# Performance work log

Measured on AMD Instinct MI355X. Metric: run time of the kernel, lower is better.

Reference implementation:

```python
import jax, jax.numpy as jnp
import numpy as np

B, T, D, H, E, K = 4, 1024, 1024, 16, 8, 2
HS = D // H
DFF = 4 * D
N = B * T
CAP_MAX = N * K // E  # static upper bound on expert capacity (all tokens non-skip)
SKIP_THR = 0.5
LN_EPS = 1e-5


def _ln(x, g, b):
    m = x.mean(-1, keepdims=True)
    v = x.var(-1, keepdims=True)  # biased, matches torch LayerNorm
    return (x - m) * jax.lax.rsqrt(v + LN_EPS) * g + b


def setup_inputs() -> dict:
    key = jax.random.key(0)
    ks = jax.random.split(key, 20)
    s = 0.02
    nrm = lambda k, shp: jax.random.normal(k, shp, dtype=jnp.float32) * s
    return {
        "x": jax.random.normal(ks[0], (B, T, D), dtype=jnp.float32),
        "noise": jax.random.normal(ks[1], (B, T, E), dtype=jnp.float32),
        "ln1_g": jnp.ones((D,), jnp.float32), "ln1_b": jnp.zeros((D,), jnp.float32),
        "wq": nrm(ks[2], (D, D)), "wk": nrm(ks[3], (D, D)), "wv": nrm(ks[4], (D, D)),
        "w_proj": nrm(ks[5], (D, D)), "b_proj": jnp.zeros((D,), jnp.float32),
        "ln2_g": jnp.ones((D,), jnp.float32), "ln2_b": jnp.zeros((D,), jnp.float32),
        "w_router": nrm(ks[6], (D, E)), "b_router": jnp.zeros((E,), jnp.float32),
        "w_noise": nrm(ks[7], (D, E)), "b_noise": jnp.zeros((E,), jnp.float32),
        "w_skip": nrm(ks[8], (D, 1)), "b_skip": jnp.zeros((1,), jnp.float32),
        "ew1": nrm(ks[9], (E, D, DFF)), "eb1": jnp.zeros((E, DFF), jnp.float32),
        "ew2": nrm(ks[10], (E, DFF, D)), "eb2": jnp.zeros((E, D), jnp.float32),
    }


def _block(x, noise, ln1_g, ln1_b, wq, wk, wv, w_proj, b_proj, ln2_g, ln2_b,
           w_router, b_router, w_noise, b_noise, w_skip, b_skip, ew1, eb1, ew2, eb2):
    # ---- multi-head causal self-attention (dropout is identity in eval) ----
    h = _ln(x, ln1_g, ln1_b)
    q = (h @ wq).reshape(B, T, H, HS)
    k = (h @ wk).reshape(B, T, H, HS)
    v = (h @ wv).reshape(B, T, H, HS)
    # NOTE: original scales by C**-0.5 with C = n_embed (not head_size)
    wei = jnp.einsum("bqhd,bkhd->bhqk", q, k) * (D ** -0.5)
    tril = jnp.tril(jnp.ones((T, T), bool))
    wei = jnp.where(tril, wei, -jnp.inf)
    wei = jax.nn.softmax(wei, axis=-1)
    attn = jnp.einsum("bhqk,bkhd->bqhd", wei, v).reshape(B, T, D)
    x1 = x + attn @ w_proj + b_proj

    # ---- cross-layer sparse MoE with skip routing ----
    h2 = _ln(x1, ln2_g, ln2_b)
    logits = h2 @ w_router + b_router                      # [B,T,E]
    noisy = logits + noise * jax.nn.softplus(h2 @ w_noise + b_noise)
    vals, idx = jax.lax.top_k(noisy, K)                    # [B,T,K]
    sparse = jnp.full_like(noisy, -jnp.inf)
    bi = jnp.arange(B)[:, None, None]
    ti = jnp.arange(T)[None, :, None]
    sparse = sparse.at[bi, ti, idx].set(vals)
    gates = jax.nn.softmax(sparse, axis=-1)                # [B,T,E]
    skip = (jax.nn.sigmoid(h2 @ w_skip + b_skip)[..., 0] > SKIP_THR)  # [B,T]

    fx = h2.reshape(N, D)
    fg = gates.reshape(N, E)
    fi = idx.reshape(N, K)
    nsk = ~skip.reshape(N)                                  # non-skip tokens
    n_ns = nsk.sum()
    capacity = (n_ns * K) // E                              # floor(tokens*K/E * 1.0)

    # per-expert dispatch with first-come capacity truncation (flat-token order)
    mask = (fi[None, :, :] == jnp.arange(E)[:, None, None]).any(-1) & nsk[None, :]  # [E,N]
    rank = jnp.cumsum(mask, axis=1) - 1                     # arrival order among non-skip
    within = mask & (rank < capacity)
    slot = jnp.where(within, rank, CAP_MAX)
    buf = jnp.full((E, CAP_MAX + 1), N, dtype=jnp.int32)
    buf = buf.at[jnp.arange(E)[:, None], slot].set(jnp.arange(N, dtype=jnp.int32)[None, :])
    tok = buf[:, :CAP_MAX]                                  # [E,CAP_MAX] token id or N (pad)
    valid = tok < N

    xp = jnp.concatenate([fx, jnp.zeros((1, D), fx.dtype)], axis=0)
    xin = xp[tok]                                           # [E,CAP_MAX,D]
    mid = jax.nn.relu(jnp.einsum("ecd,edf->ecf", xin, ew1) + eb1[:, None, :])
    yout = jnp.einsum("ecf,efd->ecd", mid, ew2) + eb2[:, None, :]
    gp = jnp.concatenate([fg, jnp.zeros((1, E), fg.dtype)], axis=0)
    gsel = gp[tok, jnp.arange(E)[:, None]]                  # [E,CAP_MAX]
    wout = yout * (gsel * valid)[..., None]

    updates = jnp.zeros((N + 1, D), fx.dtype).at[tok.reshape(-1)].add(wout.reshape(-1, D))[:N]
    moe_out = jnp.where(nsk[:, None], updates, fx).reshape(B, T, D)  # skipped tokens pass ln2(x1) through
    return x1 + moe_out


def reference(x, noise, ln1_g, ln1_b, wq, wk, wv, w_proj, b_proj, ln2_g, ln2_b,
              w_router, b_router, w_noise, b_noise, w_skip, b_skip, ew1, eb1, ew2, eb2):
    return _block(x, noise, ln1_g, ln1_b, wq, wk, wv, w_proj, b_proj, ln2_g, ln2_b,
                  w_router, b_router, w_noise, b_noise, w_skip, b_skip, ew1, eb1, ew2, eb2)
```

## Files before the change

### kernel.cpp

```cpp
#include <hip/hip_runtime.h>
#include <math.h>

#define TOK_N   4096
#define DMODEL  1024
#define NEXP    8
#define DFFD    4096
#define CAPMAX  1024

typedef __bf16 bf16x8 __attribute__((ext_vector_type(8)));
typedef __bf16 bf16x4 __attribute__((ext_vector_type(4)));
typedef float  f32x4  __attribute__((ext_vector_type(4)));

__device__ __forceinline__ f32x4 MFMA16(bf16x8 a, bf16x8 b, f32x4 c){
  return __builtin_amdgcn_mfma_f32_16x16x32_bf16(a, b, c, 0, 0, 0);
}

__device__ __forceinline__ void gl16(const __bf16* g, __bf16* l){
  __builtin_amdgcn_global_load_lds(
      (const __attribute__((address_space(1))) unsigned int*)g,
      (__attribute__((address_space(3))) unsigned int*)l, 16, 0, 0);
}

__device__ __forceinline__ float wave_sum(float x){
  #pragma unroll
  for (int o=32;o;o>>=1) x += __shfl_down(x,o);
  return x;
}

__global__ __launch_bounds__(256) void prep_kernel(
    const float* __restrict__ wq, const float* __restrict__ wk,
    const float* __restrict__ wv, const float* __restrict__ wp,
    __bf16* __restrict__ dh, __bf16* __restrict__ dl,
    const float* __restrict__ x, const float* __restrict__ g1,
    const float* __restrict__ b1, __bf16* __restrict__ hh, __bf16* __restrict__ hl)
{
  __shared__ float smem[64*65];
  int b = blockIdx.x, t = threadIdx.x;
  if (b < 1024){
    int z = b >> 8, rem = b & 255;
    int k0 = (rem >> 4) * 64, n0 = (rem & 15) * 64;
    const float* in = z==0?wq: z==1?wk: z==2?wv: wp;
    __bf16* oh = dh + (size_t)z*DMODEL*DMODEL;
    __bf16* ol = dl + (size_t)z*DMODEL*DMODEL;
    float (*tile)[65] = (float(*)[65])smem;
    #pragma unroll
    for (int i=0;i<4;i++){
      int row = (t>>4) + i*16, col = (t&15)*4;
      float4 f = *(const float4*)&in[(size_t)(k0+row)*DMODEL + n0 + col];
      tile[row][col]=f.x; tile[row][col+1]=f.y; tile[row][col+2]=f.z; tile[row][col+3]=f.w;
    }
    __syncthreads();
    #pragma unroll
    for (int i=0;i<2;i++){
      int c = t + i*256;
      int orow = c>>3, kg = (c&7)*8;
      bf16x8 hv, lv;
      #pragma unroll
      for (int u=0;u<8;u++){
        float xv = tile[kg+u][orow];
        __bf16 hb = (__bf16)xv;
        hv[u]=hb; lv[u]=(__bf16)(xv-(float)hb);
      }
      *(bf16x8*)&oh[(size_t)(n0+orow)*DMODEL + k0 + kg] = hv;
      *(bf16x8*)&ol[(size_t)(n0+orow)*DMODEL + k0 + kg] = lv;
    }
  } else {
    int n = b - 1024;
    float4 v = ((const float4*)(x + (size_t)n*DMODEL))[t];
    float s  = v.x+v.y+v.z+v.w;
    float sq = v.x*v.x+v.y*v.y+v.z*v.z+v.w*v.w;
    s = wave_sum(s); sq = wave_sum(sq);
    int lane = t & 63, wid = t >> 6;
    if (lane==0){ smem[wid]=s; smem[8+wid]=sq; }
    __syncthreads();
    if (t==0){
      float a = smem[0]+smem[1]+smem[2]+smem[3];
      float c = smem[8]+smem[9]+smem[10]+smem[11];
      float mean = a*(1.0f/DMODEL);
      float var  = c*(1.0f/DMODEL) - mean*mean;
      smem[16] = mean; smem[17] = 1.0f/sqrtf(var + 1e-5f);
    }
    __syncthreads();
    float mean = smem[16], rstd = smem[17];
    float4 g4 = ((const float4*)g1)[t];
    float4 b4 = ((const float4*)b1)[t];
    float o_[4];
    o_[0] = (v.x-mean)*rstd*g4.x + b4.x;
    o_[1] = (v.y-mean)*rstd*g4.y + b4.y;
    o_[2] = (v.z-mean)*rstd*g4.z + b4.z;
    o_[3] = (v.w-mean)*rstd*g4.w + b4.w;
    bf16x4 h4, l4;
    #pragma unroll
    for (int i=0;i<4;i++){ __bf16 hb=(__bf16)o_[i]; h4[i]=hb; l4[i]=(__bf16)(o_[i]-(float)hb); }
    *(bf16x4*)&hh[(size_t)n*DMODEL + t*4] = h4;
    *(bf16x4*)&hl[(size_t)n*DMODEL + t*4] = l4;
  }
}

__global__ __launch_bounds__(256) void ln_router_kernel(
    const float* __restrict__ p0, const float* __restrict__ p1,
    const float* __restrict__ xres, const float* __restrict__ bproj,
    const float* __restrict__ g, const float* __restrict__ b,
    __bf16* __restrict__ oh, __bf16* __restrict__ ol, float* __restrict__ out,
    const float* __restrict__ wr, const float* __restrict__ br,
    const float* __restrict__ wn, const float* __restrict__ bn,
    const float* __restrict__ wsk, const float* __restrict__ bsk,
    const float* __restrict__ noise,
    int* __restrict__ idx2, float* __restrict__ gate2, int* __restrict__ nskv)
{
  int n = blockIdx.x, t = threadIdx.x;
  size_t ro = (size_t)n*DMODEL/4 + t;
  float4 a  = ((const float4*)p0)[ro];
  float4 a1 = ((const float4*)p1)[ro];
  float4 xr = ((const float4*)xres)[ro];
  float4 bp = ((const float4*)bproj)[t];
  float4 v;
  v.x = a.x+a1.x+xr.x+bp.x; v.y = a.y+a1.y+xr.y+bp.y;
  v.z = a.z+a1.z+xr.z+bp.z; v.w = a.w+a1.w+xr.w+bp.w;
  float s  = v.x+v.y+v.z+v.w;
  float sq = v.x*v.x+v.y*v.y+v.z*v.z+v.w*v.w;
  s = wave_sum(s); sq = wave_sum(sq);
  __shared__ float r1[4], r2[4];
  __shared__ float mean_s, rstd_s, sk_s;
  int lane = t & 63, wid = t >> 6;
  if (lane==0){ r1[wid]=s; r2[wid]=sq; }
  __syncthreads();
  if (t==0){
    float aa = r1[0]+r1[1]+r1[2]+r1[3];
    float cc = r2[0]+r2[1]+r2[2]+r2[3];
    float mean = aa*(1.0f/DMODEL);
    float var  = cc*(1.0f/DMODEL) - mean*mean;
    mean_s = mean; rstd_s = 1.0f/sqrtf(var + 1e-5f);
  }
  __syncthreads();
  float mean = mean_s, rstd = rstd_s;
  float4 g4 = ((const float4*)g)[t];
  float4 b4 = ((const float4*)b)[t];
  float o_[4];
  o_[0] = (v.x-mean)*rstd*g4.x + b4.x;
  o_[1] = (v.y-mean)*rstd*g4.y + b4.y;
  o_[2] = (v.z-mean)*rstd*g4.z + b4.z;
  o_[3] = (v.w-mean)*rstd*g4.w + b4.w;
  bf16x4 h4, l4;
  #pragma unroll
  for (int i=0;i<4;i++){ __bf16 hb=(__bf16)o_[i]; h4[i]=hb; l4[i]=(__bf16)(o_[i]-(float)hb); }
  *(bf16x4*)&oh[(size_t)n*DMODEL + t*4] = h4;
  *(bf16x4*)&ol[(size_t)n*DMODEL + t*4] = l4;
  int d0 = t*4;
  const float* wrp = wr + (size_t)d0*NEXP;
  const float* wnp = wn + (size_t)d0*NEXP;
  const float* wsp = wsk + d0;
  float vals[17];
  #pragma unroll
  for (int i=0;i<17;i++) vals[i]=0.f;
  #pragma unroll
  for (int i=0;i<4;i++){
    #pragma unroll
    for (int e=0;e<NEXP;e++){
      vals[e]   += o_[i]*wrp[i*NEXP+e];
      vals[8+e] += o_[i]*wnp[i*NEXP+e];
    }
    vals[16] += o_[i]*wsp[i];
  }
  __shared__ float red[4][17];
  #pragma unroll
  for (int i=0;i<17;i++){
    float xx = wave_sum(vals[i]);
    if (lane==0) red[wid][i] = xx;
  }
  __syncthreads();
  if (t==0){
    float noisy[NEXP];
    #pragma unroll
    for (int e=0;e<NEXP;e++){
      float lr = red[0][e]+red[1][e]+red[2][e]+red[3][e] + br[e];
      float pn = red[0][8+e]+red[1][8+e]+red[2][8+e]+red[3][8+e] + bn[e];
      float sp = fmaxf(pn,0.f) + log1pf(expf(-fabsf(pn)));
      noisy[e] = lr + noise[(size_t)n*NEXP + e]*sp;
    }
    float sk = red[0][16]+red[1][16]+red[2][16]+red[3][16] + bsk[0];
    sk_s = sk;
    nskv[n] = (sk <= 0.f) ? 1 : 0;
    int i0=0; float v0=noisy[0];
    #pragma unroll
    for (int e=1;e<NEXP;e++) if (noisy[e] > v0){ v0=noisy[e]; i0=e; }
    int i1=-1; float v1=-INFINITY;
    #pragma unroll
    for (int e=0;e<NEXP;e++) if (e!=i0 && noisy[e] > v1){ v1=noisy[e]; i1=e; }
    float tt = expf(v1 - v0);
    idx2[n*2+0]=i0; idx2[n*2+1]=i1;
    gate2[n*2+0]=1.0f/(1.0f+tt); gate2[n*2+1]=tt/(1.0f+tt);
  }
  __syncthreads();
  if (sk_s > 0.f){
    v.x += o_[0]; v.y += o_[1]; v.z += o_[2]; v.w += o_[3];
  }
  ((float4*)out)[ro] = v;
}

__global__ __launch_bounds__(256) void tconv_pair(
    const float* __restrict__ ew1, const float* __restrict__ ew2,
    __bf16* __restrict__ e1T, __bf16* __restrict__ e2T, int e0)
{
  __shared__ float tile[64][65];
  int z = blockIdx.z, t = threadIdx.x;
  const float* in; __bf16* out; int K, N, k0, n0;
  if (z < 2){
    in = ew1 + (size_t)(e0+z)*DMODEL*DFFD; out = e1T + (size_t)z*DFFD*DMODEL;
    K = DMODEL; N = DFFD; k0 = blockIdx.y*64; n0 = blockIdx.x*64;
  } else {
    in = ew2 + (size_t)(e0+z-2)*DFFD*DMODEL; out = e2T + (size_t)(z-2)*DMODEL*DFFD;
    K = DFFD; N = DMODEL; k0 = blockIdx.x*64; n0 = blockIdx.y*64;
  }
  #pragma unroll
  for (int i=0;i<4;i++){
    int row = (t>>4) + i*16, col = (t&15)*4;
    float4 f = *(const float4*)&in[(size_t)(k0+row)*N + n0 + col];
    tile[row][col]=f.x; tile[row][col+1]=f.y; tile[row][col+2]=f.z; tile[row][col+3]=f.w;
  }
  __syncthreads();
  #pragma unroll
  for (int i=0;i<2;i++){
    int c = t + i*256;
    int orow = c>>3, kg = (c&7)*8;
    bf16x8 hv;
    #pragma unroll
    for (int u=0;u<8;u++) hv[u] = (__bf16)tile[kg+u][orow];
    *(bf16x8*)&out[(size_t)(n0+orow)*K + k0 + kg] = hv;
  }
}

__global__ __launch_bounds__(256) void btrans_kernel(
    const __bf16* __restrict__ ih, const __bf16* __restrict__ il, int istride, int icol0,
    __bf16* __restrict__ oh, __bf16* __restrict__ ol){
  __shared__ __bf16 th[64][72], tl[64][72];
  int r0 = blockIdx.x*64, c0 = blockIdx.y*64;
  int t = threadIdx.x;
  {
    int r = t>>2, cg = (t&3)*16;
    size_t go = (size_t)(r0+r)*istride + icol0 + c0 + cg;
    *(bf16x8*)&th[r][cg]   = *(const bf16x8*)&ih[go];
    *(bf16x8*)&th[r][cg+8] = *(const bf16x8*)&ih[go+8];
    *(bf16x8*)&tl[r][cg]   = *(const bf16x8*)&il[go];
    *(bf16x8*)&tl[r][cg+8] = *(const bf16x8*)&il[go+8];
  }
  __syncthreads();
  {
    int c = t>>2, rg = (t&3)*16;
    bf16x8 a,b,e,f;
    #pragma unroll
    for (int u=0;u<8;u++){ a[u]=th[rg+u][c]; b[u]=th[rg+8+u][c]; e[u]=tl[rg+u][c]; f[u]=tl[rg+8+u][c]; }
    size_t go = (size_t)(c0+c)*TOK_N + r0 + rg;
    *(bf16x8*)&oh[go]   = a;
    *(bf16x8*)&oh[go+8] = b;
    *(bf16x8*)&ol[go]   = e;
    *(bf16x8*)&ol[go+8] = f;
  }
}

template<int MODE, bool SPLIT>
__global__ __launch_bounds__(256) void mgemm(
    const __bf16* __restrict__ Ah, const __bf16* __restrict__ Al, int Astride,
    const __bf16* __restrict__ Bh, const __bf16* __restrict__ Bl, int Bstride,
    const float* __restrict__ bias,
    float* __restrict__ Cf, __bf16* __restrict__ Ch, __bf16* __restrict__ Cl,
    int N, int K,
    const int* __restrict__ tok, const __bf16* __restrict__ zbuf)
{
  if constexpr (MODE==2){
    int z = blockIdx.z;
    Bh  += (size_t)z*((size_t)DFFD*DMODEL);
    bias+= (size_t)z*DFFD;
    Ch  += (size_t)z*((size_t)CAPMAX*DFFD);
    tok += z*CAPMAX;
  }
  if constexpr (MODE==4){
    int pe = blockIdx.z>>2, kz = blockIdx.z&3;
    Ah  += (size_t)pe*((size_t)CAPMAX*DFFD) + kz*1024;
    Bh  += (size_t)pe*((size_t)DMODEL*DFFD) + kz*1024;
    Cf  += (size_t)blockIdx.z*((size_t)CAPMAX*DMODEL);
    tok += pe*CAPMAX;
  }
  if constexpr (MODE==5){
    int kz = blockIdx.z;
    Ah += kz*512; Al += kz*512; Bh += kz*512; Bl += kz*512;
    Cf += (size_t)kz*((size_t)TOK_N*DMODEL);
  }
  int m0 = blockIdx.y*128, n0 = blockIdx.x*128;
  if ((MODE==2||MODE==4) && tok[m0] >= TOK_N) return;
  __shared__ __align__(16) __bf16 sAh[2*128*32], sBh[2*128*32];
  __shared__ __align__(16) __bf16 sAl[SPLIT?2*128*32:8], sBl[SPLIT?2*128*32:8];
  int t = threadIdx.x, lane = t&63, w = t>>6;
  int wr = w>>1, wc = w&1, fr = lane&15, kb = lane>>4;

  const __bf16* aB[2]; const __bf16* aBl[2]; bool aval[2];
  const __bf16* bB[2]; const __bf16* bBl[2];
  #pragma unroll
  for (int j=0;j<2;j++){
    int c = j*256 + w*64 + lane;
    int row = c>>2, grp = c&3;
    int sg = grp ^ ((row>>1)&3);
    if (MODE==2){
      int token = tok[m0+row];
      if (token < TOK_N){ aB[j] = Ah + (size_t)token*Astride + sg*8; aval[j]=true; }
      else              { aB[j] = zbuf + sg*8;                       aval[j]=false; }
    } else {
      aB[j] = Ah + (size_t)(m0+row)*Astride + sg*8; aval[j]=true;
      if (SPLIT) aBl[j] = Al + (size_t)(m0+row)*Astride + sg*8;
    }
    bB[j] = Bh + (size_t)(n0+row)*Bstride + sg*8;
    if (SPLIT) bBl[j] = Bl + (size_t)(n0+row)*Bstride + sg*8;
  }

  auto stage = [&](int buf, int kt){
    int base = buf*(128*32);
    #pragma unroll
    for (int j=0;j<2;j++){
      int cb8 = base + (j*256 + w*64)*8;
      gl16(aB[j] + (aval[j]? kt : 0), &sAh[cb8]);
      gl16(bB[j] + kt, &sBh[cb8]);
      if constexpr (SPLIT){
        gl16(aBl[j] + kt, &sAl[cb8]);
        gl16(bBl[j] + kt, &sBl[cb8]);
      }
    }
  };

  f32x4 acc[4][4];
  #pragma unroll
  for (int mt=0;mt<4;mt++)
    #pragma unroll
    for (int nt=0;nt<4;nt++) acc[mt][nt] = (f32x4){0.f,0.f,0.f,0.f};

  stage(0, 0);
  __syncthreads();
  int nk = K >> 5;
  int xk = (kb ^ ((fr>>1)&3))*8;
  for (int ik=0; ik<nk; ik++){
    int cur = ik & 1;
    if (ik+1 < nk) stage(cur^1, (ik+1)<<5);
    int fb = cur*(128*32);
    bf16x8 aFh[4], bFh[4];
    #pragma unroll
    for (int mt=0;mt<4;mt++) aFh[mt] = *(const bf16x8*)&sAh[fb + (wr*64+mt*16+fr)*32 + xk];
    #pragma unroll
    for (int nt=0;nt<4;nt++) bFh[nt] = *(const bf16x8*)&sBh[fb + (wc*64+nt*16+fr)*32 + xk];
    __builtin_amdgcn_s_setprio(1);
    #pragma unroll
    for (int mt=0;mt<4;mt++)
      #pragma unroll
      for (int nt=0;nt<4;nt++)
        acc[mt][nt] = MFMA16(aFh[mt], bFh[nt], acc[mt][nt]);
    __builtin_amdgcn_s_setprio(0);
    if constexpr (SPLIT){
      bf16x8 aFl[4], bFl[4];
      #pragma unroll
      for (int mt=0;mt<4;mt++) aFl[mt] = *(const bf16x8*)&sAl[fb + (wr*64+mt*16+fr)*32 + xk];
      #pragma unroll
      for (int nt=0;nt<4;nt++) bFl[nt] = *(const bf16x8*)&sBl[fb + (wc*64+nt*16+fr)*32 + xk];
      __builtin_amdgcn_s_setprio(1);
      #pragma unroll
      for (int mt=0;mt<4;mt++)
        #pragma unroll
        for (int nt=0;nt<4;nt++){
          acc[mt][nt] = MFMA16(aFh[mt], bFl[nt], acc[mt][nt]);
          acc[mt][nt] = MFMA16(aFl[mt], bFh[nt], acc[mt][nt]);
        }
      __builtin_amdgcn_s_setprio(0);
    }
    __syncthreads();
  }

  #pragma unroll
  for (int mt=0; mt<4; mt++){
    int r0 = m0 + wr*64 + mt*16 + (lane>>4)*4;
    #pragma unroll
    for (int nt=0; nt<4; nt++){
      int col = n0 + wc*64 + nt*16 + fr;
      f32x4 v = acc[mt][nt];
      if constexpr (MODE==0){
        #pragma unroll
        for (int jj=0;jj<4;jj++){
          float val = v[jj];
          __bf16 hb = (__bf16)val;
          size_t idx = (size_t)(r0+jj)*N + col;
          Ch[idx] = hb; Cl[idx] = (__bf16)(val-(float)hb);
        }
      } else if constexpr (MODE==2){
        float bs = bias[col];
        #pragma unroll
        for (int jj=0;jj<4;jj++)
          Ch[(size_t)(r0+jj)*N + col] = (__bf16)fmaxf(v[jj]+bs, 0.f);
      } else {
        #pragma unroll
        for (int jj=0;jj<4;jj++)
          Cf[(size_t)(r0+jj)*N + col] = v[jj];
      }
    }
  }
}

__global__ __launch_bounds__(256) void sred_kernel(const float* __restrict__ yk,
    const int* __restrict__ tok, const float* __restrict__ gsel,
    const float* __restrict__ eb2, float* __restrict__ out)
{
  int r = blockIdx.x, t = threadIdx.x;
  int token = tok[r];
  if (token >= TOK_N) return;
  float g = gsel[r];
  float4 acc = ((const float4*)eb2)[t];
  #pragma unroll
  for (int z=0;z<4;z++){
    float4 p = ((const float4*)(yk + (size_t)z*CAPMAX*DMODEL + (size_t)r*DMODEL))[t];
    acc.x+=p.x; acc.y+=p.y; acc.z+=p.z; acc.w+=p.w;
  }
  float* op = out + (size_t)token*DMODEL;
  float4 o = ((float4*)op)[t];
  o.x += g*acc.x; o.y += g*acc.y; o.z += g*acc.z; o.w += g*acc.w;
  ((float4*)op)[t] = o;
}

__global__ __launch_bounds__(256) void attn_mfma_kernel(
    const __bf16* __restrict__ qkvh, const __bf16* __restrict__ qkvl,
    const __bf16* __restrict__ vth, const __bf16* __restrict__ vtl,
    __bf16* __restrict__ oh, __bf16* __restrict__ ol)
{
  __shared__ __align__(16) __bf16 Kh[2][64*64], Kl[2][64*64], Vh[2][64*64], Vl[2][64*64];
  __shared__ __align__(16) __bf16 Pt[2][4][16*64];
  int qtA = blockIdx.x, qtB = qtA + 8;
  int bh = blockIdx.y;
  int batch = bh>>4, head = bh&15;
  int t = threadIdx.x, lane = t&63, w = t>>6;
  int g = lane>>4, fr = lane&15;
  int col0 = head*64;
  size_t qbaseA = (size_t)(batch*1024 + qtA*64);
  size_t qbaseB = (size_t)(batch*1024 + qtB*64);
  const int QKS = 3*DMODEL;
  const float scale = 0.03125f;

  bf16x8 bQhA[2], bQlA[2], bQhB[2], bQlB[2];
  {
    int qrow = w*16 + fr;
    size_t rbA = (qbaseA+qrow)*QKS + col0 + g*8;
    size_t rbB = (qbaseB+qrow)*QKS + col0 + g*8;
    bQhA[0] = *(const bf16x8*)&qkvh[rbA];
    bQhA[1] = *(const bf16x8*)&qkvh[rbA+32];
    bQlA[0] = *(const bf16x8*)&qkvl[rbA];
    bQlA[1] = *(const bf16x8*)&qkvl[rbA+32];
    bQhB[0] = *(const bf16x8*)&qkvh[rbB];
    bQhB[1] = *(const bf16x8*)&qkvh[rbB+32];
    bQlB[0] = *(const bf16x8*)&qkvl[rbB];
    bQlB[1] = *(const bf16x8*)&qkvl[rbB+32];
  }

  auto stageKV = [&](int buf, int kt){
    size_t kbase = (size_t)(batch*1024 + kt*64);
    #pragma unroll
    for (int j=0;j<2;j++){
      int c = j*256 + t, row = c>>3, seg = c&7;
      int lb = (j*256 + w*64)*8;
      size_t gk = (kbase+row)*QKS + 1024 + col0 + ((seg^(row&7))*8);
      gl16(qkvh+gk, &Kh[buf][lb]);
      gl16(qkvl+gk, &Kl[buf][lb]);
      size_t gv = (size_t)(col0+row)*TOK_N + kbase + ((seg^(row&7))*8);
      gl16(vth+gv, &Vh[buf][lb]);
      gl16(vtl+gv, &Vl[buf][lb]);
    }
  };

  float mA = -INFINITY, lA = 0.f, mB = -INFINITY, lB = 0.f;
  f32x4 oA[4], oB[4];
  #pragma unroll
  for (int nt=0;nt<4;nt++){ oA[nt]=(f32x4){0.f,0.f,0.f,0.f}; oB[nt]=(f32x4){0.f,0.f,0.f,0.f}; }

  auto process = [&](int cur, bool diag, bf16x8* bQh, bf16x8* bQl,
                     float& m_, float& l_, f32x4* o_){
    int ntmax = diag ? (w+1) : 4;
    f32x4 s[4];
    #pragma unroll
    for (int nt=0;nt<4;nt++) s[nt]=(f32x4){0.f,0.f,0.f,0.f};
    __builtin_amdgcn_s_setprio(1);
    #pragma unroll
    for (int ks=0; ks<2; ks++){
      #pragma unroll
      for (int nt=0; nt<4; nt++){
        if (nt < ntmax){
          int kvr = nt*16 + fr;
          int sc_ = (ks*4 + g) ^ (kvr&7);
          bf16x8 aKh = *(const bf16x8*)&Kh[cur][kvr*64 + sc_*8];
          bf16x8 aKl = *(const bf16x8*)&Kl[cur][kvr*64 + sc_*8];
          s[nt] = MFMA16(aKh, bQh[ks], s[nt]);
          s[nt] = MFMA16(aKl, bQh[ks], s[nt]);
          s[nt] = MFMA16(aKh, bQl[ks], s[nt]);
        }
      }
    }
    __builtin_amdgcn_s_setprio(0);
    float sv[4][4];
    float mx = -INFINITY;
    int ql = w*16 + fr;
    #pragma unroll
    for (int nt=0;nt<4;nt++)
      #pragma unroll
      for (int j=0;j<4;j++){
        float xv = s[nt][j]*scale;
        if (nt >= ntmax || (diag && (nt*16 + g*4 + j) > ql)) xv = -INFINITY;
        sv[nt][j] = xv;
        mx = fmaxf(mx, xv);
      }
    mx = fmaxf(mx, __shfl_xor(mx,16));
    mx = fmaxf(mx, __shfl_xor(mx,32));
    float nm = fmaxf(m_, mx);
    float scf = __expf(m_ - nm);
    float ps = 0.f;
    #pragma unroll
    for (int nt=0;nt<4;nt++)
      #pragma unroll
      for (int j=0;j<4;j++){
        float p = __expf(sv[nt][j] - nm);
        sv[nt][j] = p;
        ps += p;
      }
    ps += __shfl_xor(ps,16);
    ps += __shfl_xor(ps,32);
    l_ = l_*scf + ps;
    m_ = nm;
    #pragma unroll
    for (int nt=0;nt<4;nt++) o_[nt] = o_[nt]*scf;
    #pragma unroll
    for (int nt=0;nt<4;nt++){
      bf16x4 hv, lv;
      #pragma unroll
      for (int j=0;j<4;j++){
        float pv = sv[nt][j];
        __bf16 hb = (__bf16)pv;
        hv[j] = hb; lv[j] = (__bf16)(pv-(float)hb);
      }
      int el = fr*64 + (((2*nt + (g>>1)) ^ (fr&7))*8) + (g&1)*4;
      *(bf16x4*)&Pt[0][w][el] = hv;
      *(bf16x4*)&Pt[1][w][el] = lv;
    }
    int ksmax = (diag && w < 2) ? 1 : 2;
    __builtin_amdgcn_s_setprio(1);
    #pragma unroll
    for (int ks=0; ks<2; ks++){
      if (ks < ksmax){
        int pc = (4*ks + g) ^ (fr&7);
        bf16x8 bPh = *(const bf16x8*)&Pt[0][w][fr*64 + pc*8];
        bf16x8 bPl = *(const bf16x8*)&Pt[1][w][fr*64 + pc*8];
        #pragma unroll
        for (int nt=0; nt<4; nt++){
          int vr = nt*16 + fr;
          int vc = (ks*4 + g) ^ (vr&7);
          bf16x8 aVh = *(const bf16x8*)&Vh[cur][vr*64 + vc*8];
          bf16x8 aVl = *(const bf16x8*)&Vl[cur][vr*64 + vc*8];
          o_[nt] = MFMA16(aVh, bPh, o_[nt]);
          o_[nt] = MFMA16(aVl, bPh, o_[nt]);
          o_[nt] = MFMA16(aVh, bPl, o_[nt]);
        }
      }
    }
    __builtin_amdgcn_s_setprio(0);
  };

  stageKV(0, 0);
  for (int kt=0; kt<=qtB; kt++){
    int cur = kt&1;
    __syncthreads();
    if (kt < qtB) stageKV(cur^1, kt+1);
    if (kt <= qtA) process(cur, kt==qtA, bQhA, bQlA, mA, lA, oA);
    process(cur, kt==qtB, bQhB, bQlB, mB, lB, oB);
  }

  auto writeOut = [&](size_t qbase, float l_, f32x4* o_){
    float inv = 1.0f/l_;
    #pragma unroll
    for (int nt=0;nt<4;nt++){
      bf16x4 hv, lv;
      #pragma unroll
      for (int j=0;j<4;j++){
        float val = o_[nt][j]*inv;
        __bf16 hb = (__bf16)val;
        hv[j] = hb; lv[j] = (__bf16)(val-(float)hb);
      }
      int el = fr*64 + (((2*nt + (g>>1)) ^ (fr&7))*8) + (g&1)*4;
      *(bf16x4*)&Pt[0][w][el] = hv;
      *(bf16x4*)&Pt[1][w][el] = lv;
    }
    #pragma unroll
    for (int r=0;r<2;r++){
      int c = r*4 + g;
      int el = fr*64 + ((c ^ (fr&7))*8);
      bf16x8 vh = *(const bf16x8*)&Pt[0][w][el];
      bf16x8 vl = *(const bf16x8*)&Pt[1][w][el];
      size_t go = (qbase + w*16 + fr)*DMODEL + col0 + c*8;
      *(bf16x8*)&oh[go] = vh;
      *(bf16x8*)&ol[go] = vl;
    }
  };
  writeOut(qbaseA, lA, oA);
  writeOut(qbaseB, lB, oB);
}

__global__ __launch_bounds__(256) void scan_kernel(const int* __restrict__ idx2,
    const float* __restrict__ gate2, const int* __restrict__ nskv,
    int* __restrict__ tok, float* __restrict__ gsel, float* __restrict__ zbuf)
{
  int t = threadIdx.x;
  for (int i=t; i<NEXP*CAPMAX; i+=256){ tok[i]=TOK_N; gsel[i]=0.f; }
  for (int i=t; i<1024; i+=256) zbuf[i]=0.f;
  __shared__ int cnts[256][NEXP];
  __shared__ int nns_part[256];
  __shared__ int cap_s;
  int loc[NEXP];
  #pragma unroll
  for (int e=0;e<NEXP;e++) loc[e]=0;
  int nn=0, base = t*16;
  for (int u=0;u<16;u++){
    int n = base+u;
    if (nskv[n]){ nn++; loc[idx2[n*2]]++; loc[idx2[n*2+1]]++; }
  }
  #pragma unroll
  for (int e=0;e<NEXP;e++) cnts[t][e]=loc[e];
  nns_part[t]=nn;
  __syncthreads();
  if (t < NEXP){ int run=0; for (int i=0;i<256;i++){ int c=cnts[i][t]; cnts[i][t]=run; run+=c; } }
  if (t == NEXP){ int sum=0; for (int i=0;i<256;i++) sum+=nns_part[i]; cap_s = sum/4; }
  __syncthreads();
  int capacity = cap_s;
  int run[NEXP];
  #pragma unroll
  for (int e=0;e<NEXP;e++) run[e]=cnts[t][e];
  for (int u=0;u<16;u++){
    int n = base+u;
    if (!nskv[n]) continue;
    #pragma unroll
    for (int kk=0;kk<2;kk++){
      int e = idx2[n*2+kk];
      int r = run[e]++;
      if (r < capacity){ tok[e*CAPMAX+r]=n; gsel[e*CAPMAX+r]=gate2[n*2+kk]; }
    }
  }
}

extern "C" void kernel_launch(void* const* d_in, const int* in_sizes, int n_in,
                              void* d_out, int out_size, void* d_ws, size_t ws_size,
                              hipStream_t stream) {
  const float* x      = (const float*)d_in[0];
  const float* noise  = (const float*)d_in[1];
  const float* ln1_g  = (const float*)d_in[2];
  const float* ln1_b  = (const float*)d_in[3];
  const float* wq     = (const float*)d_in[4];
  const float* wk     = (const float*)d_in[5];
  const float* wv     = (const float*)d_in[6];
  const float* w_proj = (const float*)d_in[7];
  const float* b_proj = (const float*)d_in[8];
  const float* ln2_g  = (const float*)d_in[9];
  const float* ln2_b  = (const float*)d_in[10];
  const float* w_rout = (const float*)d_in[11];
  const float* b_rout = (const float*)d_in[12];
  const float* w_noi  = (const float*)d_in[13];
  const float* b_noi  = (const float*)d_in[14];
  const float* w_skip = (const float*)d_in[15];
  const float* b_skip = (const float*)d_in[16];
  const float* ew1    = (const float*)d_in[17];
  const float* eb1    = (const float*)d_in[18];
  const float* ew2    = (const float*)d_in[19];
  const float* eb2    = (const float*)d_in[20];
  float* out = (float*)d_out;

  char* ws = (char*)d_ws;
  const size_t MB = 1024*1024;
  __bf16* h_hi   = (__bf16*)(ws + 0*MB);
  __bf16* h_lo   = (__bf16*)(ws + 8*MB);
  __bf16* qkv_hi = (__bf16*)(ws + 16*MB);
  __bf16* qkv_lo = (__bf16*)(ws + 40*MB);
  __bf16* wAllT_h= (__bf16*)(ws + 64*MB);
  __bf16* wAllT_l= (__bf16*)(ws + 72*MB);
  __bf16* vt_hi  = (__bf16*)(ws + 81*MB);
  __bf16* vt_lo  = (__bf16*)(ws + 89*MB);
  float*  pP     = (float*) (ws + 16*MB);
  int*   idx2  = (int*)  (ws + 96*MB);
  float* gate2 = (float*)(ws + 96*MB + 32*1024);
  int*   nskv  = (int*)  (ws + 96*MB + 64*1024);
  int*   tokb  = (int*)  (ws + 96*MB + 80*1024);
  float* gselb = (float*)(ws + 96*MB + 112*1024);
  float* zbuf  = (float*)(ws + 96*MB + 144*1024);
  __bf16* e1T_2 = (__bf16*)(ws + 16*MB);
  __bf16* e2T_2 = (__bf16*)(ws + 32*MB);
  __bf16* mid_2 = (__bf16*)(ws + 48*MB);
  float*  yk    = (float*) (ws + 64*MB);
  __bf16* ao_hi = h_hi, *ao_lo = h_lo;

  dim3 blk(256);
  prep_kernel<<<5120, blk, 0, stream>>>(wq, wk, wv, w_proj, wAllT_h, wAllT_l,
                                        x, ln1_g, ln1_b, h_hi, h_lo);
  mgemm<0,true><<<dim3(24,32), blk, 0, stream>>>(h_hi, h_lo, DMODEL, wAllT_h, wAllT_l, DMODEL,
      nullptr, nullptr, qkv_hi, qkv_lo, 3*DMODEL, DMODEL, nullptr, nullptr);
  btrans_kernel<<<dim3(64,16), blk, 0, stream>>>(qkv_hi, qkv_lo, 3*DMODEL, 2048, vt_hi, vt_lo);
  attn_mfma_kernel<<<dim3(8,64), blk, 0, stream>>>(qkv_hi, qkv_lo, vt_hi, vt_lo, ao_hi, ao_lo);
  mgemm<5,true><<<dim3(8,32,2), blk, 0, stream>>>(ao_hi, ao_lo, DMODEL,
      wAllT_h + (size_t)3*DMODEL*DMODEL, wAllT_l + (size_t)3*DMODEL*DMODEL, DMODEL,
      nullptr, pP, nullptr, nullptr, DMODEL, 512, nullptr, nullptr);
  ln_router_kernel<<<TOK_N, blk, 0, stream>>>(pP, pP + (size_t)TOK_N*DMODEL, x, b_proj,
      ln2_g, ln2_b, h_hi, h_lo, out,
      w_rout, b_rout, w_noi, b_noi, w_skip, b_skip, noise, idx2, gate2, nskv);
  scan_kernel<<<1, blk, 0, stream>>>(idx2, gate2, nskv, tokb, gselb, zbuf);
  for (int p=0; p<4; p++){
    int e0 = 2*p;
    tconv_pair<<<dim3(64,16,4), blk, 0, stream>>>(ew1, ew2, e1T_2, e2T_2, e0);
    mgemm<2,false><<<dim3(32,8,2), blk, 0, stream>>>(h_hi, nullptr, DMODEL,
        e1T_2, nullptr, DMODEL, eb1 + (size_t)e0*DFFD,
        nullptr, mid_2, nullptr, DFFD, DMODEL, tokb + e0*CAPMAX, (const __bf16*)zbuf);
    mgemm<4,false><<<dim3(8,8,8), blk, 0, stream>>>(mid_2, nullptr, DFFD,
        e2T_2, nullptr, DFFD, nullptr,
        yk, nullptr, nullptr, DMODEL, 1024, tokb + e0*CAPMAX, nullptr);
    for (int pe=0; pe<2; pe++){
      int e = e0 + pe;
      sred_kernel<<<CAPMAX, blk, 0, stream>>>(yk + (size_t)pe*4*CAPMAX*DMODEL,
          tokb + e*CAPMAX, gselb + e*CAPMAX, eb2 + (size_t)e*DMODEL, out);
    }
  }
}
```

Baseline: 606.3 us.

## Process experts in larger groups and replace per-expert scatter with per-token gather

Expert processing is batched into groups of up to 8 experts, chosen from the available workspace size, so that the weight transpose, the two expert GEMMs and the reduction each run with wider grids and fewer launches. The scan kernel now also records, for each token, which expert slots it occupies. A per-token gather kernel replaces the per-expert scatter kernels, reading the split-K partials and adding gated outputs in one read-modify-write of each output row. Larger groups need much more workspace, and the gather launches one block per token even when most tokens are absent from the current group.

```diff
diff --git a/kernel.cpp b/kernel.cpp
--- a/kernel.cpp
+++ b/kernel.cpp
@@ -198,18 +198,18 @@
   ((float4*)out)[ro] = v;
 }
 
-__global__ __launch_bounds__(256) void tconv_pair(
+__global__ __launch_bounds__(256) void tconv_group(
     const float* __restrict__ ew1, const float* __restrict__ ew2,
-    __bf16* __restrict__ e1T, __bf16* __restrict__ e2T, int e0)
+    __bf16* __restrict__ e1T, __bf16* __restrict__ e2T, int e0, int G)
 {
   __shared__ float tile[64][65];
   int z = blockIdx.z, t = threadIdx.x;
   const float* in; __bf16* out; int K, N, k0, n0;
-  if (z < 2){
+  if (z < G){
     in = ew1 + (size_t)(e0+z)*DMODEL*DFFD; out = e1T + (size_t)z*DFFD*DMODEL;
     K = DMODEL; N = DFFD; k0 = blockIdx.y*64; n0 = blockIdx.x*64;
   } else {
-    in = ew2 + (size_t)(e0+z-2)*DFFD*DMODEL; out = e2T + (size_t)(z-2)*DMODEL*DFFD;
+    in = ew2 + (size_t)(e0+z-G)*DFFD*DMODEL; out = e2T + (size_t)(z-G)*DMODEL*DFFD;
     K = DFFD; N = DMODEL; k0 = blockIdx.x*64; n0 = blockIdx.y*64;
   }
   #pragma unroll
@@ -275,11 +275,11 @@
     tok += z*CAPMAX;
   }
   if constexpr (MODE==4){
-    int pe = blockIdx.z>>2, kz = blockIdx.z&3;
-    Ah  += (size_t)pe*((size_t)CAPMAX*DFFD) + kz*1024;
-    Bh  += (size_t)pe*((size_t)DMODEL*DFFD) + kz*1024;
+    int ge = blockIdx.z>>2, kz = blockIdx.z&3;
+    Ah  += (size_t)ge*((size_t)CAPMAX*DFFD) + kz*1024;
+    Bh  += (size_t)ge*((size_t)DMODEL*DFFD) + kz*1024;
     Cf  += (size_t)blockIdx.z*((size_t)CAPMAX*DMODEL);
-    tok += pe*CAPMAX;
+    tok += ge*CAPMAX;
   }
   if constexpr (MODE==5){
     int kz = blockIdx.z;
@@ -400,24 +400,32 @@
   }
 }
 
-__global__ __launch_bounds__(256) void sred_kernel(const float* __restrict__ yk,
-    const int* __restrict__ tok, const float* __restrict__ gsel,
-    const float* __restrict__ eb2, float* __restrict__ out)
+__global__ __launch_bounds__(256) void gather_kernel(const float* __restrict__ yk,
+    const int* __restrict__ tsrc, const float* __restrict__ gselb,
+    const float* __restrict__ eb2, int e0, int G, float* __restrict__ out)
 {
-  int r = blockIdx.x, t = threadIdx.x;
-  int token = tok[r];
-  if (token >= TOK_N) return;
-  float g = gsel[r];
-  float4 acc = ((const float4*)eb2)[t];
-  #pragma unroll
-  for (int z=0;z<4;z++){
-    float4 p = ((const float4*)(yk + (size_t)z*CAPMAX*DMODEL + (size_t)r*DMODEL))[t];
-    acc.x+=p.x; acc.y+=p.y; acc.z+=p.z; acc.w+=p.w;
-  }
-  float* op = out + (size_t)token*DMODEL;
-  float4 o = ((float4*)op)[t];
-  o.x += g*acc.x; o.y += g*acc.y; o.z += g*acc.z; o.w += g*acc.w;
-  ((float4*)op)[t] = o;
+  int n = blockIdx.x, t = threadIdx.x;
+  int s0 = tsrc[n*2], s1 = tsrc[n*2+1];
+  float4 o; bool any = false;
+  #pragma unroll
+  for (int kk=0; kk<2; kk++){
+    int src = kk ? s1 : s0;
+    if (src < 0) continue;
+    int e = src >> 10;
+    int ge = e - e0;
+    if (ge < 0 || ge >= G) continue;
+    int r = src & (CAPMAX-1);
+    if (!any){ o = ((const float4*)(out + (size_t)n*DMODEL))[t]; any = true; }
+    float g = gselb[src];
+    float4 acc = ((const float4*)(eb2 + (size_t)e*DMODEL))[t];
+    #pragma unroll
+    for (int z=0; z<4; z++){
+      float4 p = ((const float4*)(yk + ((size_t)(ge*4+z)*CAPMAX + r)*DMODEL))[t];
+      acc.x+=p.x; acc.y+=p.y; acc.z+=p.z; acc.w+=p.w;
+    }
+    o.x += g*acc.x; o.y += g*acc.y; o.z += g*acc.z; o.w += g*acc.w;
+  }
+  if (any) ((float4*)(out + (size_t)n*DMODEL))[t] = o;
 }
 
 __global__ __launch_bounds__(256) void attn_mfma_kernel(
@@ -604,10 +612,12 @@
 
 __global__ __launch_bounds__(256) void scan_kernel(const int* __restrict__ idx2,
     const float* __restrict__ gate2, const int* __restrict__ nskv,
-    int* __restrict__ tok, float* __restrict__ gsel, float* __restrict__ zbuf)
+    int* __restrict__ tok, float* __restrict__ gsel, float* __restrict__ zbuf,
+    int* __restrict__ tsrc)
 {
   int t = threadIdx.x;
   for (int i=t; i<NEXP*CAPMAX; i+=256){ tok[i]=TOK_N; gsel[i]=0.f; }
+  for (int i=t; i<2*TOK_N; i+=256) tsrc[i] = -1;
   for (int i=t; i<1024; i+=256) zbuf[i]=0.f;
   __shared__ int cnts[256][NEXP];
   __shared__ int nns_part[256];
@@ -638,7 +648,10 @@
     for (int kk=0;kk<2;kk++){
       int e = idx2[n*2+kk];
       int r = run[e]++;
-      if (r < capacity){ tok[e*CAPMAX+r]=n; gsel[e*CAPMAX+r]=gate2[n*2+kk]; }
+      if (r < capacity){
+        tok[e*CAPMAX+r]=n; gsel[e*CAPMAX+r]=gate2[n*2+kk];
+        tsrc[n*2+kk] = e*CAPMAX + r;
+      }
     }
   }
 }
@@ -680,17 +693,28 @@
   __bf16* vt_hi  = (__bf16*)(ws + 81*MB);
   __bf16* vt_lo  = (__bf16*)(ws + 89*MB);
   float*  pP     = (float*) (ws + 16*MB);
-  int*   idx2  = (int*)  (ws + 96*MB);
-  float* gate2 = (float*)(ws + 96*MB + 32*1024);
-  int*   nskv  = (int*)  (ws + 96*MB + 64*1024);
-  int*   tokb  = (int*)  (ws + 96*MB + 80*1024);
-  float* gselb = (float*)(ws + 96*MB + 112*1024);
-  float* zbuf  = (float*)(ws + 96*MB + 144*1024);
-  __bf16* e1T_2 = (__bf16*)(ws + 16*MB);
-  __bf16* e2T_2 = (__bf16*)(ws + 32*MB);
-  __bf16* mid_2 = (__bf16*)(ws + 48*MB);
-  float*  yk    = (float*) (ws + 64*MB);
   __bf16* ao_hi = h_hi, *ao_lo = h_lo;
+
+  int G; size_t off_mid, off_yk, off_e1, off_e2, off_meta;
+  if (ws_size >= (size_t)338*MB){
+    G = 8;  off_mid = 16;  off_yk = 80;  off_e1 = 208; off_e2 = 272; off_meta = 336;
+  } else if (ws_size >= (size_t)178*MB){
+    G = 4;  off_mid = 16;  off_yk = 48;  off_e1 = 112; off_e2 = 144; off_meta = 176;
+  } else {
+    G = 2;  off_e1 = 16;  off_e2 = 32;  off_mid = 48;  off_yk = 64;  off_meta = 96;
+  }
+  __bf16* e1T = (__bf16*)(ws + off_e1*MB);
+  __bf16* e2T = (__bf16*)(ws + off_e2*MB);
+  __bf16* mid = (__bf16*)(ws + off_mid*MB);
+  float*  yk  = (float*) (ws + off_yk*MB);
+  char* meta = ws + off_meta*MB;
+  int*   idx2  = (int*)  (meta);
+  float* gate2 = (float*)(meta + 32*1024);
+  int*   nskv  = (int*)  (meta + 64*1024);
+  int*   tokb  = (int*)  (meta + 80*1024);
+  float* gselb = (float*)(meta + 112*1024);
+  float* zbuf  = (float*)(meta + 144*1024);
+  int*   tsrc  = (int*)  (meta + 160*1024);
 
   dim3 blk(256);
   prep_kernel<<<5120, blk, 0, stream>>>(wq, wk, wv, w_proj, wAllT_h, wAllT_l,
@@ -705,20 +729,17 @@
   ln_router_kernel<<<TOK_N, blk, 0, stream>>>(pP, pP + (size_t)TOK_N*DMODEL, x, b_proj,
       ln2_g, ln2_b, h_hi, h_lo, out,
       w_rout, b_rout, w_noi, b_noi, w_skip, b_skip, noise, idx2, gate2, nskv);
-  scan_kernel<<<1, blk, 0, stream>>>(idx2, gate2, nskv, tokb, gselb, zbuf);
-  for (int p=0; p<4; p++){
-    int e0 = 2*p;
-    tconv_pair<<<dim3(64,16,4), blk, 0, stream>>>(ew1, ew2, e1T_2, e2T_2, e0);
-    mgemm<2,false><<<dim3(32,8,2), blk, 0, stream>>>(h_hi, nullptr, DMODEL,
-        e1T_2, nullptr, DMODEL, eb1 + (size_t)e0*DFFD,
-        nullptr, mid_2, nullptr, DFFD, DMODEL, tokb + e0*CAPMAX, (const __bf16*)zbuf);
-    mgemm<4,false><<<dim3(8,8,8), blk, 0, stream>>>(mid_2, nullptr, DFFD,
-        e2T_2, nullptr, DFFD, nullptr,
+  scan_kernel<<<1, blk, 0, stream>>>(idx2, gate2, nskv, tokb, gselb, zbuf, tsrc);
+  int ngrp = NEXP / G;
+  for (int grp=0; grp<ngrp; grp++){
+    int e0 = grp*G;
+    tconv_group<<<dim3(64,16,2*G), blk, 0, stream>>>(ew1, ew2, e1T, e2T, e0, G);
+    mgemm<2,false><<<dim3(32,8,G), blk, 0, stream>>>(h_hi, nullptr, DMODEL,
+        e1T, nullptr, DMODEL, eb1 + (size_t)e0*DFFD,
+        nullptr, mid, nullptr, DFFD, DMODEL, tokb + e0*CAPMAX, (const __bf16*)zbuf);
+    mgemm<4,false><<<dim3(8,8,4*G), blk, 0, stream>>>(mid, nullptr, DFFD,
+        e2T, nullptr, DFFD, nullptr,
         yk, nullptr, nullptr, DMODEL, 1024, tokb + e0*CAPMAX, nullptr);
-    for (int pe=0; pe<2; pe++){
-      int e = e0 + pe;
-      sred_kernel<<<CAPMAX, blk, 0, stream>>>(yk + (size_t)pe*4*CAPMAX*DMODEL,
-          tokb + e*CAPMAX, gselb + e*CAPMAX, eb2 + (size_t)e*DMODEL, out);
-    }
-  }
-}
+    gather_kernel<<<TOK_N, blk, 0, stream>>>(yk, tsrc, gselb, eb2, e0, G, out);
+  }
+}
```

New measurement: 529.1 us. 1.15x faster.
